# Performance work log

Measured on AMD Instinct MI355X. Metric: run time of the kernel, lower is better.

## Reference

```python
import jax, jax.numpy as jnp
import numpy as np
from jax import lax

BATCH = 524288
N_LINKS = 8   # body 0 = fixed base, bodies 1..7 have revolute joints
N_DOFS = 7
G = 9.81      # base linear acceleration z-component encodes gravity

def _skew(v):
    x, y, z = v[..., 0], v[..., 1], v[..., 2]
    o = jnp.zeros_like(x)
    return jnp.stack([jnp.stack([o, -z, y], -1),
                      jnp.stack([z, o, -x], -1),
                      jnp.stack([-y, x, o], -1)], -2)

def _rodrigues(axis, theta):
    # rotation about unit axis by theta; broadcasts axis[...,3] with theta[...]
    K = _skew(axis)
    s = jnp.sin(theta)[..., None, None]
    c = jnp.cos(theta)[..., None, None]
    I = jnp.eye(3, dtype=jnp.result_type(theta))
    return I + s * K + (1.0 - c) * (K @ K)

def setup_inputs():
    key = jax.random.key(0)
    ks = jax.random.split(key, 10)
    q = jax.random.normal(ks[0], (BATCH, N_DOFS), jnp.float32)
    qd = jax.random.normal(ks[1], (BATCH, N_DOFS), jnp.float32)
    qdd_des = jax.random.normal(ks[2], (BATCH, N_DOFS), jnp.float32)
    # fixed (URDF) joint transforms: valid random rotations + link-offset translations
    ax = jax.random.normal(ks[3], (N_LINKS, 3), jnp.float32)
    ax = ax / jnp.linalg.norm(ax, axis=-1, keepdims=True)
    ang = jax.random.uniform(ks[4], (N_LINKS,), jnp.float32, -1.0, 1.0)
    rot_fix = _rodrigues(ax, ang)
    trans_fix = jax.random.uniform(ks[5], (N_LINKS, 3), jnp.float32, -0.25, 0.25)
    # single-coordinate joint axes with signs, as in URDF revolute joints
    joint_axes = jnp.asarray([[0, 0, 1], [0, 1, 0], [0, 0, 1], [0, -1, 0],
                              [0, 0, 1], [0, 1, 0], [0, 0, 1]], jnp.float32)
    mass = jax.random.uniform(ks[6], (N_LINKS,), jnp.float32, 0.5, 4.0)
    com = 0.05 * jax.random.normal(ks[7], (N_LINKS, 3), jnp.float32)
    A = 0.1 * jax.random.normal(ks[8], (N_LINKS, 3, 3), jnp.float32)
    inertia = A @ jnp.swapaxes(A, -1, -2) + 0.05 * jnp.eye(3, dtype=jnp.float32)
    damping = jax.random.uniform(ks[9], (N_DOFS,), jnp.float32, 0.01, 0.2)
    return dict(q=q, qd=qd, qdd_des=qdd_des, rot_fix=rot_fix, trans_fix=trans_fix,
                joint_axes=joint_axes, mass=mass, com=com, inertia=inertia, damping=damping)

def reference(q, qd, qdd_des, rot_fix, trans_fix, joint_axes, mass, com, inertia, damping):
    # Batched recursive Newton-Euler inverse dynamics over a serial chain,
    # matching DifferentiableRobotModel.compute_inverse_dynamics (gravity+damping on).
    B, D = q.shape
    # joint pose of body i(=dof j+1): rotation = rot_fix[i] @ R(axis_j, q_j), translation = trans_fix[i]
    Rq = _rodrigues(joint_axes[None, :, :], q)                     # [B,D,3,3]
    R = jnp.einsum('dij,bdjk->dbik', rot_fix[1:], Rq)              # [D,B,3,3]
    p = trans_fix[1:]                                              # [D,3]
    jv = qd.T[:, :, None] * joint_axes[:, None, :]                 # [D,B,3] joint angular vel
    ja = qdd_des.T[:, :, None] * joint_axes[:, None, :]            # [D,B,3] joint angular acc

    z = jnp.zeros((B, 3), q.dtype)
    base_acc_lin = z.at[:, 2].set(G)

    # forward pass: propagate spatial velocity/acceleration root -> leaf
    def fwd_step(carry, xs):
        vl, va, al, aa = carry
        Ri, pi, jvi, jai = xs
        Rt = jnp.swapaxes(Ri, -1, -2)
        pinv = -jnp.einsum('bij,j->bi', Rt, pi)
        # SpatialMotionVec.transform with inverse joint pose (Rt, pinv)
        va_n = jnp.einsum('bij,bj->bi', Rt, va)
        vl_n = jnp.einsum('bij,bj->bi', Rt, vl) + jnp.cross(pinv, va_n)
        va_i = va_n + jvi
        vl_i = vl_n
        aa_n = jnp.einsum('bij,bj->bi', Rt, aa)
        al_n = jnp.einsum('bij,bj->bi', Rt, al) + jnp.cross(pinv, aa_n)
        # acc = parent_acc(transformed) + joint_acc + vel x joint_vel (joint_vel.lin = 0)
        aa_i = aa_n + jai + jnp.cross(va_i, jvi)
        al_i = al_n + jnp.cross(vl_i, jvi)
        new = (vl_i, va_i, al_i, aa_i)
        return new, new

    _, (vl, va, al, aa) = lax.scan(fwd_step, (z, z, base_acc_lin, z), (R, p, jv, ja))

    # spatial inertia (about body frame origin) acting on motion vectors
    m = mass[1:, None, None]                                       # [D,1,1]
    mc = mass[1:, None] * com[1:]                                  # [D,3]
    cs = _skew(com[1:])
    Io = inertia[1:] + mass[1:, None, None] * (cs @ jnp.swapaxes(cs, -1, -2))

    def imul(lin, ang):
        return (m * lin + jnp.cross(ang, mc[:, None, :]),
                jnp.einsum('dij,dbj->dbi', Io, ang) + jnp.cross(mc[:, None, :], lin))

    Ia_l, Ia_a = imul(al, aa)
    Iv_l, Iv_a = imul(vl, va)
    # f = I*acc + vel x* (I*vel)
    f_l = Ia_l + jnp.cross(va, Iv_l)
    f_a = Ia_a + jnp.cross(va, Iv_a) + jnp.cross(vl, Iv_l)

    # backward pass: accumulate forces leaf -> root; tau_j = f.ang . axis_j
    def bwd_step(carry, xs):
        cl, ca = carry
        fl, fa, Ri, pi, axi = xs
        tl = fl + cl
        ta = fa + ca
        tau = jnp.einsum('bi,i->b', ta, axi)
        # SpatialForceVec.transform with joint pose (Ri, pi)
        nl = jnp.einsum('bij,bj->bi', Ri, tl)
        na = jnp.einsum('bij,bj->bi', Ri, ta) + jnp.cross(pi[None, :], nl)
        return (nl, na), tau

    _, taus = lax.scan(bwd_step, (z, z), (f_l, f_a, R, p, joint_axes), reverse=True)
    return jnp.swapaxes(taus, 0, 1) + damping[None, :] * qd        # [B,D]
```

## Files before the change

kernel.cpp:

```cpp
#include <hip/hip_runtime.h>

#define NDOF 7
#define BLK 256
#define CST_STRIDE 24
#define CST_TOT (NDOF * CST_STRIDE)
#define NPARK 5
#define FREC 33

struct V3 { float x, y, z; };
__device__ __forceinline__ V3 operator+(V3 a, V3 b) { return {a.x + b.x, a.y + b.y, a.z + b.z}; }
__device__ __forceinline__ V3 operator-(V3 a, V3 b) { return {a.x - b.x, a.y - b.y, a.z - b.z}; }
__device__ __forceinline__ V3 operator*(float s, V3 a) { return {s * a.x, s * a.y, s * a.z}; }
__device__ __forceinline__ V3 cross(V3 a, V3 b) {
    return {a.y * b.z - a.z * b.y, a.z * b.x - a.x * b.z, a.x * b.y - a.y * b.x};
}
__device__ __forceinline__ float dot(V3 a, V3 b) { return a.x * b.x + a.y * b.y + a.z * b.z; }

__global__ void rnea_prep(const float* __restrict__ rot_fix,
                          const float* __restrict__ trans_fix,
                          const float* __restrict__ mass_g,
                          const float* __restrict__ com_g,
                          const float* __restrict__ inertia_g,
                          const float* __restrict__ damping_g,
                          float* __restrict__ cst) {
    const int d = threadIdx.x;
    if (d >= NDOF) return;
    float* o = cst + d * CST_STRIDE;
    const float* F = rot_fix + (1 + d) * 9;
#pragma unroll
    for (int j = 0; j < 3; j++)
#pragma unroll
        for (int i = 0; i < 3; i++) o[j * 3 + i] = F[i * 3 + j];
#pragma unroll
    for (int i = 0; i < 3; i++) o[9 + i] = trans_fix[(1 + d) * 3 + i];
    const float m = mass_g[1 + d];
    const float c0 = com_g[(1 + d) * 3 + 0];
    const float c1 = com_g[(1 + d) * 3 + 1];
    const float c2 = com_g[(1 + d) * 3 + 2];
    const float* I = inertia_g + (1 + d) * 9;
    o[12] = I[0] + m * (c1 * c1 + c2 * c2);
    o[13] = I[1] - m * c0 * c1;
    o[14] = I[2] - m * c0 * c2;
    o[15] = I[4] + m * (c0 * c0 + c2 * c2);
    o[16] = I[5] - m * c1 * c2;
    o[17] = I[8] + m * (c0 * c0 + c1 * c1);
    o[18] = m;
    o[19] = m * c0;
    o[20] = m * c1;
    o[21] = m * c2;
    o[22] = damping_g[d];
    o[23] = 0.f;
}

template <int AX>
__device__ __forceinline__ void make_R(V3 Fc0, V3 Fc1, V3 Fc2, float s, float c,
                                       V3& R0, V3& R1, V3& R2) {
    if (AX == 0) {
        R0 = c * Fc0 + s * Fc1;
        R1 = c * Fc1 - s * Fc0;
        R2 = Fc2;
    } else if (AX == 1) {
        R0 = c * Fc0 - s * Fc2;
        R1 = Fc1;
        R2 = s * Fc0 + c * Fc2;
    } else {
        R0 = c * Fc0 + s * Fc2;
        R1 = Fc1;
        R2 = c * Fc2 - s * Fc0;
    }
}

template <int AX>
__device__ __forceinline__ void fwd_step(const float4* C4, float s, float c,
                                         float qd, float qdd, V3& vl, V3& va, V3& al,
                                         V3& aa, V3& fl, V3& fa) {
    const float4 A0 = C4[0], A1 = C4[1], A2 = C4[2], A3 = C4[3], A4 = C4[4], A5 = C4[5];
    const V3 Fc0{A0.x, A0.y, A0.z};
    const V3 Fc1{A0.w, A1.x, A1.y};
    const V3 Fc2{A1.z, A1.w, A2.x};
    const V3 p{A2.y, A2.z, A2.w};
    const float I00 = A3.x, I01 = A3.y, I02 = A3.z, I11 = A3.w, I12 = A4.x, I22 = A4.y;
    const float m = A4.z;
    const V3 mc{A4.w, A5.x, A5.y};

    V3 R0, R1, R2;
    make_R<AX>(Fc0, Fc1, Fc2, s, c, R0, R1, R2);

    V3 w1 = vl + cross(va, p);
    V3 w2 = al + cross(aa, p);
    V3 nvl{dot(R0, w1), dot(R1, w1), dot(R2, w1)};
    V3 nva{dot(R0, va), dot(R1, va), dot(R2, va)};
    V3 nal{dot(R0, w2), dot(R1, w2), dot(R2, w2)};
    V3 naa{dot(R0, aa), dot(R1, aa), dot(R2, aa)};

    if (AX == 0) {
        va = {nva.x, nva.y, nva.z + qd};
        aa = {naa.x + va.y * qd, naa.y - va.x * qd, naa.z + qdd};
        vl = nvl;
        al = {nal.x + vl.y * qd, nal.y - vl.x * qd, nal.z};
    } else if (AX == 1) {
        va = {nva.x, nva.y + qd, nva.z};
        aa = {naa.x - va.z * qd, naa.y + qdd, naa.z + va.x * qd};
        vl = nvl;
        al = {nal.x - vl.z * qd, nal.y, nal.z + vl.x * qd};
    } else {
        va = {nva.x, nva.y - qd, nva.z};
        aa = {naa.x + va.z * qd, naa.y - qdd, naa.z - va.x * qd};
        vl = nvl;
        al = {nal.x + vl.z * qd, nal.y, nal.z - vl.x * qd};
    }

    V3 Ial = m * al + cross(aa, mc);
    V3 Iaa = V3{I00 * aa.x + I01 * aa.y + I02 * aa.z,
                I01 * aa.x + I11 * aa.y + I12 * aa.z,
                I02 * aa.x + I12 * aa.y + I22 * aa.z} + cross(mc, al);
    V3 Ivl = m * vl + cross(va, mc);
    V3 Iva = V3{I00 * va.x + I01 * va.y + I02 * va.z,
                I01 * va.x + I11 * va.y + I12 * va.z,
                I02 * va.x + I12 * va.y + I22 * va.z} + cross(mc, vl);
    fl = Ial + cross(va, Ivl);
    fa = Iaa + cross(va, Iva) + cross(vl, Ivl);
}

template <int AX>
__device__ __forceinline__ float bwd_core(const float4* C4, float s, float c,
                                          V3 fl, V3 fa, V3& cl, V3& ca) {
    const float4 A0 = C4[0], A1 = C4[1], A2 = C4[2];
    const V3 Fc0{A0.x, A0.y, A0.z};
    const V3 Fc1{A0.w, A1.x, A1.y};
    const V3 Fc2{A1.z, A1.w, A2.x};
    const V3 p{A2.y, A2.z, A2.w};

    V3 tl = fl + cl;
    V3 ta = fa + ca;
    float tau;
    if (AX == 0) tau = ta.z;
    else if (AX == 1) tau = ta.y;
    else tau = -ta.y;

    V3 R0, R1, R2;
    make_R<AX>(Fc0, Fc1, Fc2, s, c, R0, R1, R2);
    V3 nl = tl.x * R0 + tl.y * R1 + tl.z * R2;
    V3 na = ta.x * R0 + ta.y * R1 + ta.z * R2 + cross(p, nl);
    cl = nl;
    ca = na;
    return tau;
}

__global__ __launch_bounds__(BLK) void rnea_main(
    const float* __restrict__ q_g, const float* __restrict__ qd_g,
    const float* __restrict__ qdd_g, const float* __restrict__ cst,
    float* __restrict__ out, int nbatch) {
    __shared__ __align__(16) float sC[CST_TOT];
    __shared__ float sF[BLK * FREC];
    const int t = threadIdx.x;
    const int row = blockIdx.x * BLK + t;

    if (t < CST_TOT) sC[t] = cst[t];
    __syncthreads();

    const bool ok = row < nbatch;
    const size_t go = (size_t)row * NDOF;
    float qd[NDOF], ss[NDOF], cc[NDOF];
    V3 cl{0.f, 0.f, 0.f}, ca{0.f, 0.f, 0.f};
    float tau5 = 0.f, tau6 = 0.f;
    float* frec = sF + t * FREC;
    const float4* C4 = reinterpret_cast<const float4*>(sC);

    if (ok) {
        float q[NDOF], qdd[NDOF];
#pragma unroll
        for (int d = 0; d < NDOF; d++) q[d] = q_g[go + d];
#pragma unroll
        for (int d = 0; d < NDOF; d++) qd[d] = qd_g[go + d];
#pragma unroll
        for (int d = 0; d < NDOF; d++) qdd[d] = qdd_g[go + d];
#pragma unroll
        for (int d = 0; d < NDOF; d++) { ss[d] = __sinf(q[d]); cc[d] = __cosf(q[d]); }

        V3 vl{0.f, 0.f, 0.f}, va{0.f, 0.f, 0.f}, al{0.f, 0.f, 9.81f}, aa{0.f, 0.f, 0.f};
        V3 fl, fa;
        fwd_step<0>(C4 + 0 * 6, ss[0], cc[0], qd[0], qdd[0], vl, va, al, aa, fl, fa);
        frec[0] = fl.x; frec[1] = fl.y; frec[2] = fl.z; frec[3] = fa.x; frec[4] = fa.y; frec[5] = fa.z;
        fwd_step<1>(C4 + 1 * 6, ss[1], cc[1], qd[1], qdd[1], vl, va, al, aa, fl, fa);
        frec[6] = fl.x; frec[7] = fl.y; frec[8] = fl.z; frec[9] = fa.x; frec[10] = fa.y; frec[11] = fa.z;
        fwd_step<0>(C4 + 2 * 6, ss[2], cc[2], qd[2], qdd[2], vl, va, al, aa, fl, fa);
        frec[12] = fl.x; frec[13] = fl.y; frec[14] = fl.z; frec[15] = fa.x; frec[16] = fa.y; frec[17] = fa.z;
        fwd_step<2>(C4 + 3 * 6, ss[3], cc[3], qd[3], qdd[3], vl, va, al, aa, fl, fa);
        frec[18] = fl.x; frec[19] = fl.y; frec[20] = fl.z; frec[21] = fa.x; frec[22] = fa.y; frec[23] = fa.z;
        fwd_step<0>(C4 + 4 * 6, ss[4], cc[4], qd[4], qdd[4], vl, va, al, aa, fl, fa);
        frec[24] = fl.x; frec[25] = fl.y; frec[26] = fl.z; frec[27] = fa.x; frec[28] = fa.y; frec[29] = fa.z;

        V3 fl5, fa5, fl6, fa6;
        fwd_step<1>(C4 + 5 * 6, ss[5], cc[5], qd[5], qdd[5], vl, va, al, aa, fl5, fa5);
        fwd_step<0>(C4 + 6 * 6, ss[6], cc[6], qd[6], qdd[6], vl, va, al, aa, fl6, fa6);
        tau6 = bwd_core<0>(C4 + 6 * 6, ss[6], cc[6], fl6, fa6, cl, ca);
        tau5 = bwd_core<1>(C4 + 5 * 6, ss[5], cc[5], fl5, fa5, cl, ca);
    }

    __syncthreads();

    if (ok) {
        float tau[NDOF];
        tau[6] = tau6;
        tau[5] = tau5;
        V3 fl, fa;
        fl = {frec[24], frec[25], frec[26]}; fa = {frec[27], frec[28], frec[29]};
        tau[4] = bwd_core<0>(C4 + 4 * 6, ss[4], cc[4], fl, fa, cl, ca);
        fl = {frec[18], frec[19], frec[20]}; fa = {frec[21], frec[22], frec[23]};
        tau[3] = bwd_core<2>(C4 + 3 * 6, ss[3], cc[3], fl, fa, cl, ca);
        fl = {frec[12], frec[13], frec[14]}; fa = {frec[15], frec[16], frec[17]};
        tau[2] = bwd_core<0>(C4 + 2 * 6, ss[2], cc[2], fl, fa, cl, ca);
        fl = {frec[6], frec[7], frec[8]}; fa = {frec[9], frec[10], frec[11]};
        tau[1] = bwd_core<1>(C4 + 1 * 6, ss[1], cc[1], fl, fa, cl, ca);
        fl = {frec[0], frec[1], frec[2]}; fa = {frec[3], frec[4], frec[5]};
        tau[0] = bwd_core<0>(C4 + 0 * 6, ss[0], cc[0], fl, fa, cl, ca);

#pragma unroll
        for (int d = 0; d < NDOF; d++)
            out[go + d] = tau[d] + sC[d * CST_STRIDE + 22] * qd[d];
    }
}

extern "C" void kernel_launch(void* const* d_in, const int* in_sizes, int n_in,
                              void* d_out, int out_size, void* d_ws, size_t ws_size,
                              hipStream_t stream) {
    const float* q = (const float*)d_in[0];
    const float* qd = (const float*)d_in[1];
    const float* qdd = (const float*)d_in[2];
    const float* rot_fix = (const float*)d_in[3];
    const float* trans_fix = (const float*)d_in[4];
    const float* mass = (const float*)d_in[6];
    const float* com = (const float*)d_in[7];
    const float* inertia = (const float*)d_in[8];
    const float* damping = (const float*)d_in[9];
    float* out = (float*)d_out;
    float* cst = (float*)d_ws;

    const int n_elem = in_sizes[0];
    const int B = n_elem / NDOF;
    const int grid = (B + BLK - 1) / BLK;

    rnea_prep<<<1, 64, 0, stream>>>(rot_fix, trans_fix, mass, com, inertia, damping, cst);
    rnea_main<<<grid, BLK, 0, stream>>>(q, qd, qdd, cst, out, B);
}
```

Measured before the change: 123.4 us.

## Replace stored-force backward pass with eager per-link force propagation

Each link's spatial force is now propagated toward the root as soon as the forward step produces it, and its contribution is added to every ancestor's torque. This removes the per-thread shared-memory record of forces (about 33 KB per block), so occupancy can rise. The cost is quadratic work: 21 transform steps instead of 7. The separate prep kernel is also merged into the main kernel, with each block computing the link constants into shared memory, which drops one launch.

Measured after the change: 148.0 us. 1.2x slower.

```diff
diff --git a/kernel.cpp b/kernel.cpp
--- a/kernel.cpp
+++ b/kernel.cpp
@@ -4,8 +4,6 @@
 #define BLK 256
 #define CST_STRIDE 24
 #define CST_TOT (NDOF * CST_STRIDE)
-#define NPARK 5
-#define FREC 33
 
 struct V3 { float x, y, z; };
 __device__ __forceinline__ V3 operator+(V3 a, V3 b) { return {a.x + b.x, a.y + b.y, a.z + b.z}; }
@@ -15,42 +13,6 @@
     return {a.y * b.z - a.z * b.y, a.z * b.x - a.x * b.z, a.x * b.y - a.y * b.x};
 }
 __device__ __forceinline__ float dot(V3 a, V3 b) { return a.x * b.x + a.y * b.y + a.z * b.z; }
-
-__global__ void rnea_prep(const float* __restrict__ rot_fix,
-                          const float* __restrict__ trans_fix,
-                          const float* __restrict__ mass_g,
-                          const float* __restrict__ com_g,
-                          const float* __restrict__ inertia_g,
-                          const float* __restrict__ damping_g,
-                          float* __restrict__ cst) {
-    const int d = threadIdx.x;
-    if (d >= NDOF) return;
-    float* o = cst + d * CST_STRIDE;
-    const float* F = rot_fix + (1 + d) * 9;
-#pragma unroll
-    for (int j = 0; j < 3; j++)
-#pragma unroll
-        for (int i = 0; i < 3; i++) o[j * 3 + i] = F[i * 3 + j];
-#pragma unroll
-    for (int i = 0; i < 3; i++) o[9 + i] = trans_fix[(1 + d) * 3 + i];
-    const float m = mass_g[1 + d];
-    const float c0 = com_g[(1 + d) * 3 + 0];
-    const float c1 = com_g[(1 + d) * 3 + 1];
-    const float c2 = com_g[(1 + d) * 3 + 2];
-    const float* I = inertia_g + (1 + d) * 9;
-    o[12] = I[0] + m * (c1 * c1 + c2 * c2);
-    o[13] = I[1] - m * c0 * c1;
-    o[14] = I[2] - m * c0 * c2;
-    o[15] = I[4] + m * (c0 * c0 + c2 * c2);
-    o[16] = I[5] - m * c1 * c2;
-    o[17] = I[8] + m * (c0 * c0 + c1 * c1);
-    o[18] = m;
-    o[19] = m * c0;
-    o[20] = m * c1;
-    o[21] = m * c2;
-    o[22] = damping_g[d];
-    o[23] = 0.f;
-}
 
 template <int AX>
 __device__ __forceinline__ void make_R(V3 Fc0, V3 Fc1, V3 Fc2, float s, float c,
@@ -123,52 +85,73 @@
 }
 
 template <int AX>
-__device__ __forceinline__ float bwd_core(const float4* C4, float s, float c,
-                                          V3 fl, V3 fa, V3& cl, V3& ca) {
+__device__ __forceinline__ void prop_step(const float4* C4, float s, float c,
+                                          V3& tl, V3& ta) {
     const float4 A0 = C4[0], A1 = C4[1], A2 = C4[2];
     const V3 Fc0{A0.x, A0.y, A0.z};
     const V3 Fc1{A0.w, A1.x, A1.y};
     const V3 Fc2{A1.z, A1.w, A2.x};
     const V3 p{A2.y, A2.z, A2.w};
-
-    V3 tl = fl + cl;
-    V3 ta = fa + ca;
-    float tau;
-    if (AX == 0) tau = ta.z;
-    else if (AX == 1) tau = ta.y;
-    else tau = -ta.y;
-
     V3 R0, R1, R2;
     make_R<AX>(Fc0, Fc1, Fc2, s, c, R0, R1, R2);
     V3 nl = tl.x * R0 + tl.y * R1 + tl.z * R2;
     V3 na = ta.x * R0 + ta.y * R1 + ta.z * R2 + cross(p, nl);
-    cl = nl;
-    ca = na;
-    return tau;
+    tl = nl;
+    ta = na;
+}
+
+template <int AX>
+__device__ __forceinline__ float taudot(V3 ta) {
+    if (AX == 0) return ta.z;
+    else if (AX == 1) return ta.y;
+    else return -ta.y;
 }
 
 __global__ __launch_bounds__(BLK) void rnea_main(
     const float* __restrict__ q_g, const float* __restrict__ qd_g,
-    const float* __restrict__ qdd_g, const float* __restrict__ cst,
+    const float* __restrict__ qdd_g,
+    const float* __restrict__ rot_fix, const float* __restrict__ trans_fix,
+    const float* __restrict__ mass_g, const float* __restrict__ com_g,
+    const float* __restrict__ inertia_g, const float* __restrict__ damping_g,
     float* __restrict__ out, int nbatch) {
     __shared__ __align__(16) float sC[CST_TOT];
-    __shared__ float sF[BLK * FREC];
     const int t = threadIdx.x;
     const int row = blockIdx.x * BLK + t;
-
-    if (t < CST_TOT) sC[t] = cst[t];
-    __syncthreads();
-
     const bool ok = row < nbatch;
     const size_t go = (size_t)row * NDOF;
-    float qd[NDOF], ss[NDOF], cc[NDOF];
-    V3 cl{0.f, 0.f, 0.f}, ca{0.f, 0.f, 0.f};
-    float tau5 = 0.f, tau6 = 0.f;
-    float* frec = sF + t * FREC;
-    const float4* C4 = reinterpret_cast<const float4*>(sC);
-
+
+    if (t < NDOF) {
+        const int d = t;
+        float* o = sC + d * CST_STRIDE;
+        const float* F = rot_fix + (1 + d) * 9;
+#pragma unroll
+        for (int j = 0; j < 3; j++)
+#pragma unroll
+            for (int i = 0; i < 3; i++) o[j * 3 + i] = F[i * 3 + j];
+#pragma unroll
+        for (int i = 0; i < 3; i++) o[9 + i] = trans_fix[(1 + d) * 3 + i];
+        const float m = mass_g[1 + d];
+        const float c0 = com_g[(1 + d) * 3 + 0];
+        const float c1 = com_g[(1 + d) * 3 + 1];
+        const float c2 = com_g[(1 + d) * 3 + 2];
+        const float* I = inertia_g + (1 + d) * 9;
+        o[12] = I[0] + m * (c1 * c1 + c2 * c2);
+        o[13] = I[1] - m * c0 * c1;
+        o[14] = I[2] - m * c0 * c2;
+        o[15] = I[4] + m * (c0 * c0 + c2 * c2);
+        o[16] = I[5] - m * c1 * c2;
+        o[17] = I[8] + m * (c0 * c0 + c1 * c1);
+        o[18] = m;
+        o[19] = m * c0;
+        o[20] = m * c1;
+        o[21] = m * c2;
+        o[22] = damping_g[d];
+        o[23] = 0.f;
+    }
+
+    float qd[NDOF], ss[NDOF], cc[NDOF], qdd[NDOF];
     if (ok) {
-        float q[NDOF], qdd[NDOF];
+        float q[NDOF];
 #pragma unroll
         for (int d = 0; d < NDOF; d++) q[d] = q_g[go + d];
 #pragma unroll
@@ -177,45 +160,65 @@
         for (int d = 0; d < NDOF; d++) qdd[d] = qdd_g[go + d];
 #pragma unroll
         for (int d = 0; d < NDOF; d++) { ss[d] = __sinf(q[d]); cc[d] = __cosf(q[d]); }
-
+    }
+
+    __syncthreads();
+
+    if (ok) {
+        const float4* C4 = reinterpret_cast<const float4*>(sC);
         V3 vl{0.f, 0.f, 0.f}, va{0.f, 0.f, 0.f}, al{0.f, 0.f, 9.81f}, aa{0.f, 0.f, 0.f};
-        V3 fl, fa;
+        V3 fl, fa, tl, ta;
+        float tau0, tau1, tau2, tau3, tau4, tau5, tau6;
+
         fwd_step<0>(C4 + 0 * 6, ss[0], cc[0], qd[0], qdd[0], vl, va, al, aa, fl, fa);
-        frec[0] = fl.x; frec[1] = fl.y; frec[2] = fl.z; frec[3] = fa.x; frec[4] = fa.y; frec[5] = fa.z;
+        tau0 = taudot<0>(fa);
+
         fwd_step<1>(C4 + 1 * 6, ss[1], cc[1], qd[1], qdd[1], vl, va, al, aa, fl, fa);
-        frec[6] = fl.x; frec[7] = fl.y; frec[8] = fl.z; frec[9] = fa.x; frec[10] = fa.y; frec[11] = fa.z;
+        tau1 = taudot<1>(fa);
+        tl = fl; ta = fa;
+        prop_step<1>(C4 + 1 * 6, ss[1], cc[1], tl, ta); tau0 += taudot<0>(ta);
+
         fwd_step<0>(C4 + 2 * 6, ss[2], cc[2], qd[2], qdd[2], vl, va, al, aa, fl, fa);
-        frec[12] = fl.x; frec[13] = fl.y; frec[14] = fl.z; frec[15] = fa.x; frec[16] = fa.y; frec[17] = fa.z;
+        tau2 = taudot<0>(fa);
+        tl = fl; ta = fa;
+        prop_step<0>(C4 + 2 * 6, ss[2], cc[2], tl, ta); tau1 += taudot<1>(ta);
+        prop_step<1>(C4 + 1 * 6, ss[1], cc[1], tl, ta); tau0 += taudot<0>(ta);
+
         fwd_step<2>(C4 + 3 * 6, ss[3], cc[3], qd[3], qdd[3], vl, va, al, aa, fl, fa);
-        frec[18] = fl.x; frec[19] = fl.y; frec[20] = fl.z; frec[21] = fa.x; frec[22] = fa.y; frec[23] = fa.z;
+        tau3 = taudot<2>(fa);
+        tl = fl; ta = fa;
+        prop_step<2>(C4 + 3 * 6, ss[3], cc[3], tl, ta); tau2 += taudot<0>(ta);
+        prop_step<0>(C4 + 2 * 6, ss[2], cc[2], tl, ta); tau1 += taudot<1>(ta);
+        prop_step<1>(C4 + 1 * 6, ss[1], cc[1], tl, ta); tau0 += taudot<0>(ta);
+
         fwd_step<0>(C4 + 4 * 6, ss[4], cc[4], qd[4], qdd[4], vl, va, al, aa, fl, fa);
-        frec[24] = fl.x; frec[25] = fl.y; frec[26] = fl.z; frec[27] = fa.x; frec[28] = fa.y; frec[29] = fa.z;
-
-        V3 fl5, fa5, fl6, fa6;
-        fwd_step<1>(C4 + 5 * 6, ss[5], cc[5], qd[5], qdd[5], vl, va, al, aa, fl5, fa5);
-        fwd_step<0>(C4 + 6 * 6, ss[6], cc[6], qd[6], qdd[6], vl, va, al, aa, fl6, fa6);
-        tau6 = bwd_core<0>(C4 + 6 * 6, ss[6], cc[6], fl6, fa6, cl, ca);
-        tau5 = bwd_core<1>(C4 + 5 * 6, ss[5], cc[5], fl5, fa5, cl, ca);
-    }
-
-    __syncthreads();
-
-    if (ok) {
-        float tau[NDOF];
-        tau[6] = tau6;
-        tau[5] = tau5;
-        V3 fl, fa;
-        fl = {frec[24], frec[25], frec[26]}; fa = {frec[27], frec[28], frec[29]};
-        tau[4] = bwd_core<0>(C4 + 4 * 6, ss[4], cc[4], fl, fa, cl, ca);
-        fl = {frec[18], frec[19], frec[20]}; fa = {frec[21], frec[22], frec[23]};
-        tau[3] = bwd_core<2>(C4 + 3 * 6, ss[3], cc[3], fl, fa, cl, ca);
-        fl = {frec[12], frec[13], frec[14]}; fa = {frec[15], frec[16], frec[17]};
-        tau[2] = bwd_core<0>(C4 + 2 * 6, ss[2], cc[2], fl, fa, cl, ca);
-        fl = {frec[6], frec[7], frec[8]}; fa = {frec[9], frec[10], frec[11]};
-        tau[1] = bwd_core<1>(C4 + 1 * 6, ss[1], cc[1], fl, fa, cl, ca);
-        fl = {frec[0], frec[1], frec[2]}; fa = {frec[3], frec[4], frec[5]};
-        tau[0] = bwd_core<0>(C4 + 0 * 6, ss[0], cc[0], fl, fa, cl, ca);
-
+        tau4 = taudot<0>(fa);
+        tl = fl; ta = fa;
+        prop_step<0>(C4 + 4 * 6, ss[4], cc[4], tl, ta); tau3 += taudot<2>(ta);
+        prop_step<2>(C4 + 3 * 6, ss[3], cc[3], tl, ta); tau2 += taudot<0>(ta);
+        prop_step<0>(C4 + 2 * 6, ss[2], cc[2], tl, ta); tau1 += taudot<1>(ta);
+        prop_step<1>(C4 + 1 * 6, ss[1], cc[1], tl, ta); tau0 += taudot<0>(ta);
+
+        fwd_step<1>(C4 + 5 * 6, ss[5], cc[5], qd[5], qdd[5], vl, va, al, aa, fl, fa);
+        tau5 = taudot<1>(fa);
+        tl = fl; ta = fa;
+        prop_step<1>(C4 + 5 * 6, ss[5], cc[5], tl, ta); tau4 += taudot<0>(ta);
+        prop_step<0>(C4 + 4 * 6, ss[4], cc[4], tl, ta); tau3 += taudot<2>(ta);
+        prop_step<2>(C4 + 3 * 6, ss[3], cc[3], tl, ta); tau2 += taudot<0>(ta);
+        prop_step<0>(C4 + 2 * 6, ss[2], cc[2], tl, ta); tau1 += taudot<1>(ta);
+        prop_step<1>(C4 + 1 * 6, ss[1], cc[1], tl, ta); tau0 += taudot<0>(ta);
+
+        fwd_step<0>(C4 + 6 * 6, ss[6], cc[6], qd[6], qdd[6], vl, va, al, aa, fl, fa);
+        tau6 = taudot<0>(fa);
+        tl = fl; ta = fa;
+        prop_step<0>(C4 + 6 * 6, ss[6], cc[6], tl, ta); tau5 += taudot<1>(ta);
+        prop_step<1>(C4 + 5 * 6, ss[5], cc[5], tl, ta); tau4 += taudot<0>(ta);
+        prop_step<0>(C4 + 4 * 6, ss[4], cc[4], tl, ta); tau3 += taudot<2>(ta);
+        prop_step<2>(C4 + 3 * 6, ss[3], cc[3], tl, ta); tau2 += taudot<0>(ta);
+        prop_step<0>(C4 + 2 * 6, ss[2], cc[2], tl, ta); tau1 += taudot<1>(ta);
+        prop_step<1>(C4 + 1 * 6, ss[1], cc[1], tl, ta); tau0 += taudot<0>(ta);
+
+        float tau[NDOF] = {tau0, tau1, tau2, tau3, tau4, tau5, tau6};
 #pragma unroll
         for (int d = 0; d < NDOF; d++)
             out[go + d] = tau[d] + sC[d * CST_STRIDE + 22] * qd[d];
@@ -235,12 +238,11 @@
     const float* inertia = (const float*)d_in[8];
     const float* damping = (const float*)d_in[9];
     float* out = (float*)d_out;
-    float* cst = (float*)d_ws;
 
     const int n_elem = in_sizes[0];
     const int B = n_elem / NDOF;
     const int grid = (B + BLK - 1) / BLK;
 
-    rnea_prep<<<1, 64, 0, stream>>>(rot_fix, trans_fix, mass, com, inertia, damping, cst);
-    rnea_main<<<grid, BLK, 0, stream>>>(q, qd, qdd, cst, out, B);
-}
+    rnea_main<<<grid, BLK, 0, stream>>>(q, qd, qdd, rot_fix, trans_fix, mass, com,
+                                        inertia, damping, out, B);
+}
```

## Keep forward forces in registers and read constants directly from global memory

Applied to the files above, without the earlier changes.

Removes the shared-memory staging of the per-link constants and the per-thread shared-memory spill of forward-pass forces. All seven links' spatial forces now stay in registers, and constants are read through uniform global loads that the compiler can turn into scalar loads. This drops the LDS traffic and both block barriers, and clamps out-of-range rows instead of branching around the compute. The cost is higher VGPR pressure, which may lower occupancy or cause spills.

Result: slower. 134.5 us (+9.0%).

```diff
diff --git a/kernel.cpp b/kernel.cpp
--- a/kernel.cpp
+++ b/kernel.cpp
@@ -4,8 +4,6 @@
 #define BLK 256
 #define CST_STRIDE 24
 #define CST_TOT (NDOF * CST_STRIDE)
-#define NPARK 5
-#define FREC 33
 
 struct V3 { float x, y, z; };
 __device__ __forceinline__ V3 operator+(V3 a, V3 b) { return {a.x + b.x, a.y + b.y, a.z + b.z}; }
@@ -71,17 +69,16 @@
 }
 
 template <int AX>
-__device__ __forceinline__ void fwd_step(const float4* C4, float s, float c,
+__device__ __forceinline__ void fwd_step(const float* __restrict__ C, float s, float c,
                                          float qd, float qdd, V3& vl, V3& va, V3& al,
                                          V3& aa, V3& fl, V3& fa) {
-    const float4 A0 = C4[0], A1 = C4[1], A2 = C4[2], A3 = C4[3], A4 = C4[4], A5 = C4[5];
-    const V3 Fc0{A0.x, A0.y, A0.z};
-    const V3 Fc1{A0.w, A1.x, A1.y};
-    const V3 Fc2{A1.z, A1.w, A2.x};
-    const V3 p{A2.y, A2.z, A2.w};
-    const float I00 = A3.x, I01 = A3.y, I02 = A3.z, I11 = A3.w, I12 = A4.x, I22 = A4.y;
-    const float m = A4.z;
-    const V3 mc{A4.w, A5.x, A5.y};
+    const V3 Fc0{C[0], C[1], C[2]};
+    const V3 Fc1{C[3], C[4], C[5]};
+    const V3 Fc2{C[6], C[7], C[8]};
+    const V3 p{C[9], C[10], C[11]};
+    const float I00 = C[12], I01 = C[13], I02 = C[14], I11 = C[15], I12 = C[16], I22 = C[17];
+    const float m = C[18];
+    const V3 mc{C[19], C[20], C[21]};
 
     V3 R0, R1, R2;
     make_R<AX>(Fc0, Fc1, Fc2, s, c, R0, R1, R2);
@@ -123,13 +120,12 @@
 }
 
 template <int AX>
-__device__ __forceinline__ float bwd_core(const float4* C4, float s, float c,
+__device__ __forceinline__ float bwd_core(const float* __restrict__ C, float s, float c,
                                           V3 fl, V3 fa, V3& cl, V3& ca) {
-    const float4 A0 = C4[0], A1 = C4[1], A2 = C4[2];
-    const V3 Fc0{A0.x, A0.y, A0.z};
-    const V3 Fc1{A0.w, A1.x, A1.y};
-    const V3 Fc2{A1.z, A1.w, A2.x};
-    const V3 p{A2.y, A2.z, A2.w};
+    const V3 Fc0{C[0], C[1], C[2]};
+    const V3 Fc1{C[3], C[4], C[5]};
+    const V3 Fc2{C[6], C[7], C[8]};
+    const V3 p{C[9], C[10], C[11]};
 
     V3 tl = fl + cl;
     V3 ta = fa + ca;
@@ -151,74 +147,46 @@
     const float* __restrict__ q_g, const float* __restrict__ qd_g,
     const float* __restrict__ qdd_g, const float* __restrict__ cst,
     float* __restrict__ out, int nbatch) {
-    __shared__ __align__(16) float sC[CST_TOT];
-    __shared__ float sF[BLK * FREC];
     const int t = threadIdx.x;
     const int row = blockIdx.x * BLK + t;
-
-    if (t < CST_TOT) sC[t] = cst[t];
-    __syncthreads();
-
-    const bool ok = row < nbatch;
-    const size_t go = (size_t)row * NDOF;
-    float qd[NDOF], ss[NDOF], cc[NDOF];
+    const int rowc = row < nbatch ? row : (nbatch - 1);
+    const size_t go = (size_t)rowc * NDOF;
+
+    float q[NDOF], qd[NDOF], qdd[NDOF], ss[NDOF], cc[NDOF];
+#pragma unroll
+    for (int d = 0; d < NDOF; d++) q[d] = q_g[go + d];
+#pragma unroll
+    for (int d = 0; d < NDOF; d++) qd[d] = qd_g[go + d];
+#pragma unroll
+    for (int d = 0; d < NDOF; d++) qdd[d] = qdd_g[go + d];
+#pragma unroll
+    for (int d = 0; d < NDOF; d++) { ss[d] = __sinf(q[d]); cc[d] = __cosf(q[d]); }
+
+    V3 vl{0.f, 0.f, 0.f}, va{0.f, 0.f, 0.f}, al{0.f, 0.f, 9.81f}, aa{0.f, 0.f, 0.f};
+    V3 fl0, fa0, fl1, fa1, fl2, fa2, fl3, fa3, fl4, fa4, fl5, fa5, fl6, fa6;
+
+    fwd_step<0>(cst + 0 * CST_STRIDE, ss[0], cc[0], qd[0], qdd[0], vl, va, al, aa, fl0, fa0);
+    fwd_step<1>(cst + 1 * CST_STRIDE, ss[1], cc[1], qd[1], qdd[1], vl, va, al, aa, fl1, fa1);
+    fwd_step<0>(cst + 2 * CST_STRIDE, ss[2], cc[2], qd[2], qdd[2], vl, va, al, aa, fl2, fa2);
+    fwd_step<2>(cst + 3 * CST_STRIDE, ss[3], cc[3], qd[3], qdd[3], vl, va, al, aa, fl3, fa3);
+    fwd_step<0>(cst + 4 * CST_STRIDE, ss[4], cc[4], qd[4], qdd[4], vl, va, al, aa, fl4, fa4);
+    fwd_step<1>(cst + 5 * CST_STRIDE, ss[5], cc[5], qd[5], qdd[5], vl, va, al, aa, fl5, fa5);
+    fwd_step<0>(cst + 6 * CST_STRIDE, ss[6], cc[6], qd[6], qdd[6], vl, va, al, aa, fl6, fa6);
+
     V3 cl{0.f, 0.f, 0.f}, ca{0.f, 0.f, 0.f};
-    float tau5 = 0.f, tau6 = 0.f;
-    float* frec = sF + t * FREC;
-    const float4* C4 = reinterpret_cast<const float4*>(sC);
-
-    if (ok) {
-        float q[NDOF], qdd[NDOF];
-#pragma unroll
-        for (int d = 0; d < NDOF; d++) q[d] = q_g[go + d];
-#pragma unroll
-        for (int d = 0; d < NDOF; d++) qd[d] = qd_g[go + d];
-#pragma unroll
-        for (int d = 0; d < NDOF; d++) qdd[d] = qdd_g[go + d];
-#pragma unroll
-        for (int d = 0; d < NDOF; d++) { ss[d] = __sinf(q[d]); cc[d] = __cosf(q[d]); }
-
-        V3 vl{0.f, 0.f, 0.f}, va{0.f, 0.f, 0.f}, al{0.f, 0.f, 9.81f}, aa{0.f, 0.f, 0.f};
-        V3 fl, fa;
-        fwd_step<0>(C4 + 0 * 6, ss[0], cc[0], qd[0], qdd[0], vl, va, al, aa, fl, fa);
-        frec[0] = fl.x; frec[1] = fl.y; frec[2] = fl.z; frec[3] = fa.x; frec[4] = fa.y; frec[5] = fa.z;
-        fwd_step<1>(C4 + 1 * 6, ss[1], cc[1], qd[1], qdd[1], vl, va, al, aa, fl, fa);
-        frec[6] = fl.x; frec[7] = fl.y; frec[8] = fl.z; frec[9] = fa.x; frec[10] = fa.y; frec[11] = fa.z;
-        fwd_step<0>(C4 + 2 * 6, ss[2], cc[2], qd[2], qdd[2], vl, va, al, aa, fl, fa);
-        frec[12] = fl.x; frec[13] = fl.y; frec[14] = fl.z; frec[15] = fa.x; frec[16] = fa.y; frec[17] = fa.z;
-        fwd_step<2>(C4 + 3 * 6, ss[3], cc[3], qd[3], qdd[3], vl, va, al, aa, fl, fa);
-        frec[18] = fl.x; frec[19] = fl.y; frec[20] = fl.z; frec[21] = fa.x; frec[22] = fa.y; frec[23] = fa.z;
-        fwd_step<0>(C4 + 4 * 6, ss[4], cc[4], qd[4], qdd[4], vl, va, al, aa, fl, fa);
-        frec[24] = fl.x; frec[25] = fl.y; frec[26] = fl.z; frec[27] = fa.x; frec[28] = fa.y; frec[29] = fa.z;
-
-        V3 fl5, fa5, fl6, fa6;
-        fwd_step<1>(C4 + 5 * 6, ss[5], cc[5], qd[5], qdd[5], vl, va, al, aa, fl5, fa5);
-        fwd_step<0>(C4 + 6 * 6, ss[6], cc[6], qd[6], qdd[6], vl, va, al, aa, fl6, fa6);
-        tau6 = bwd_core<0>(C4 + 6 * 6, ss[6], cc[6], fl6, fa6, cl, ca);
-        tau5 = bwd_core<1>(C4 + 5 * 6, ss[5], cc[5], fl5, fa5, cl, ca);
-    }
-
-    __syncthreads();
-
-    if (ok) {
-        float tau[NDOF];
-        tau[6] = tau6;
-        tau[5] = tau5;
-        V3 fl, fa;
-        fl = {frec[24], frec[25], frec[26]}; fa = {frec[27], frec[28], frec[29]};
-        tau[4] = bwd_core<0>(C4 + 4 * 6, ss[4], cc[4], fl, fa, cl, ca);
-        fl = {frec[18], frec[19], frec[20]}; fa = {frec[21], frec[22], frec[23]};
-        tau[3] = bwd_core<2>(C4 + 3 * 6, ss[3], cc[3], fl, fa, cl, ca);
-        fl = {frec[12], frec[13], frec[14]}; fa = {frec[15], frec[16], frec[17]};
-        tau[2] = bwd_core<0>(C4 + 2 * 6, ss[2], cc[2], fl, fa, cl, ca);
-        fl = {frec[6], frec[7], frec[8]}; fa = {frec[9], frec[10], frec[11]};
-        tau[1] = bwd_core<1>(C4 + 1 * 6, ss[1], cc[1], fl, fa, cl, ca);
-        fl = {frec[0], frec[1], frec[2]}; fa = {frec[3], frec[4], frec[5]};
-        tau[0] = bwd_core<0>(C4 + 0 * 6, ss[0], cc[0], fl, fa, cl, ca);
-
+    float tau[NDOF];
+    tau[6] = bwd_core<0>(cst + 6 * CST_STRIDE, ss[6], cc[6], fl6, fa6, cl, ca);
+    tau[5] = bwd_core<1>(cst + 5 * CST_STRIDE, ss[5], cc[5], fl5, fa5, cl, ca);
+    tau[4] = bwd_core<0>(cst + 4 * CST_STRIDE, ss[4], cc[4], fl4, fa4, cl, ca);
+    tau[3] = bwd_core<2>(cst + 3 * CST_STRIDE, ss[3], cc[3], fl3, fa3, cl, ca);
+    tau[2] = bwd_core<0>(cst + 2 * CST_STRIDE, ss[2], cc[2], fl2, fa2, cl, ca);
+    tau[1] = bwd_core<1>(cst + 1 * CST_STRIDE, ss[1], cc[1], fl1, fa1, cl, ca);
+    tau[0] = bwd_core<0>(cst + 0 * CST_STRIDE, ss[0], cc[0], fl0, fa0, cl, ca);
+
+    if (row < nbatch) {
 #pragma unroll
         for (int d = 0; d < NDOF; d++)
-            out[go + d] = tau[d] + sC[d * CST_STRIDE + 22] * qd[d];
+            out[go + d] = tau[d] + cst[d * CST_STRIDE + 22] * qd[d];
     }
 }
 
```

## Fuse constant prep into main kernel and roll RNEA loops with SoA force spill

Applied to the files above, without the earlier changes.

Removes the separate prep kernel so each block computes the per-link constants into shared memory, saving one launch. The forward and backward recursions become non-unrolled loops with a runtime axis switch. All seven link forces are spilled to a structure-of-arrays shared buffer to avoid bank conflicts, and q/qd are reloaded and sin/cos recomputed in the backward pass instead of being held in registers. This aims to cut register pressure and raise occupancy, at the cost of extra global reloads, duplicated transcendental work, branch overhead and a larger shared-memory footprint.

New measurement: 126.8 us. 2.7% more time.

```diff
diff --git a/kernel.cpp b/kernel.cpp
--- a/kernel.cpp
+++ b/kernel.cpp
@@ -4,8 +4,7 @@
 #define BLK 256
 #define CST_STRIDE 24
 #define CST_TOT (NDOF * CST_STRIDE)
-#define NPARK 5
-#define FREC 33
+#define SF_FLOATS (NDOF * 6 * BLK)
 
 struct V3 { float x, y, z; };
 __device__ __forceinline__ V3 operator+(V3 a, V3 b) { return {a.x + b.x, a.y + b.y, a.z + b.z}; }
@@ -15,42 +14,6 @@
     return {a.y * b.z - a.z * b.y, a.z * b.x - a.x * b.z, a.x * b.y - a.y * b.x};
 }
 __device__ __forceinline__ float dot(V3 a, V3 b) { return a.x * b.x + a.y * b.y + a.z * b.z; }
-
-__global__ void rnea_prep(const float* __restrict__ rot_fix,
-                          const float* __restrict__ trans_fix,
-                          const float* __restrict__ mass_g,
-                          const float* __restrict__ com_g,
-                          const float* __restrict__ inertia_g,
-                          const float* __restrict__ damping_g,
-                          float* __restrict__ cst) {
-    const int d = threadIdx.x;
-    if (d >= NDOF) return;
-    float* o = cst + d * CST_STRIDE;
-    const float* F = rot_fix + (1 + d) * 9;
-#pragma unroll
-    for (int j = 0; j < 3; j++)
-#pragma unroll
-        for (int i = 0; i < 3; i++) o[j * 3 + i] = F[i * 3 + j];
-#pragma unroll
-    for (int i = 0; i < 3; i++) o[9 + i] = trans_fix[(1 + d) * 3 + i];
-    const float m = mass_g[1 + d];
-    const float c0 = com_g[(1 + d) * 3 + 0];
-    const float c1 = com_g[(1 + d) * 3 + 1];
-    const float c2 = com_g[(1 + d) * 3 + 2];
-    const float* I = inertia_g + (1 + d) * 9;
-    o[12] = I[0] + m * (c1 * c1 + c2 * c2);
-    o[13] = I[1] - m * c0 * c1;
-    o[14] = I[2] - m * c0 * c2;
-    o[15] = I[4] + m * (c0 * c0 + c2 * c2);
-    o[16] = I[5] - m * c1 * c2;
-    o[17] = I[8] + m * (c0 * c0 + c1 * c1);
-    o[18] = m;
-    o[19] = m * c0;
-    o[20] = m * c1;
-    o[21] = m * c2;
-    o[22] = damping_g[d];
-    o[23] = 0.f;
-}
 
 template <int AX>
 __device__ __forceinline__ void make_R(V3 Fc0, V3 Fc1, V3 Fc2, float s, float c,
@@ -147,78 +110,92 @@
     return tau;
 }
 
+__device__ __forceinline__ int axid(int d) { return (d & 1) ? ((d == 3) ? 2 : 1) : 0; }
+
 __global__ __launch_bounds__(BLK) void rnea_main(
     const float* __restrict__ q_g, const float* __restrict__ qd_g,
-    const float* __restrict__ qdd_g, const float* __restrict__ cst,
+    const float* __restrict__ qdd_g,
+    const float* __restrict__ rot_fix, const float* __restrict__ trans_fix,
+    const float* __restrict__ mass_g, const float* __restrict__ com_g,
+    const float* __restrict__ inertia_g, const float* __restrict__ damping_g,
     float* __restrict__ out, int nbatch) {
     __shared__ __align__(16) float sC[CST_TOT];
-    __shared__ float sF[BLK * FREC];
+    __shared__ float sF[SF_FLOATS];
     const int t = threadIdx.x;
     const int row = blockIdx.x * BLK + t;
-
-    if (t < CST_TOT) sC[t] = cst[t];
+    const bool ok = row < nbatch;
+    const int rc = ok ? row : (nbatch - 1);
+    const size_t go = (size_t)rc * NDOF;
+
+    if (t < NDOF) {
+        const int d = t;
+        float* o = sC + d * CST_STRIDE;
+        const float* F = rot_fix + (1 + d) * 9;
+#pragma unroll
+        for (int j = 0; j < 3; j++)
+#pragma unroll
+            for (int i = 0; i < 3; i++) o[j * 3 + i] = F[i * 3 + j];
+#pragma unroll
+        for (int i = 0; i < 3; i++) o[9 + i] = trans_fix[(1 + d) * 3 + i];
+        const float m = mass_g[1 + d];
+        const float c0 = com_g[(1 + d) * 3 + 0];
+        const float c1 = com_g[(1 + d) * 3 + 1];
+        const float c2 = com_g[(1 + d) * 3 + 2];
+        const float* I = inertia_g + (1 + d) * 9;
+        o[12] = I[0] + m * (c1 * c1 + c2 * c2);
+        o[13] = I[1] - m * c0 * c1;
+        o[14] = I[2] - m * c0 * c2;
+        o[15] = I[4] + m * (c0 * c0 + c2 * c2);
+        o[16] = I[5] - m * c1 * c2;
+        o[17] = I[8] + m * (c0 * c0 + c1 * c1);
+        o[18] = m;
+        o[19] = m * c0;
+        o[20] = m * c1;
+        o[21] = m * c2;
+        o[22] = damping_g[d];
+        o[23] = 0.f;
+    }
     __syncthreads();
 
-    const bool ok = row < nbatch;
-    const size_t go = (size_t)row * NDOF;
-    float qd[NDOF], ss[NDOF], cc[NDOF];
+    V3 vl{0.f, 0.f, 0.f}, va{0.f, 0.f, 0.f}, al{0.f, 0.f, 9.81f}, aa{0.f, 0.f, 0.f};
+    float q_n = q_g[go], qd_n = qd_g[go], qdd_n = qdd_g[go];
+#pragma clang loop unroll(disable)
+    for (int d = 0; d < NDOF; ++d) {
+        const float qc = q_n, qdc = qd_n, qddc = qdd_n;
+        const int dn = (d < NDOF - 1) ? (d + 1) : (NDOF - 1);
+        q_n = q_g[go + dn];
+        qd_n = qd_g[go + dn];
+        qdd_n = qdd_g[go + dn];
+        const float s = __sinf(qc), c = __cosf(qc);
+        const float4* C4 = reinterpret_cast<const float4*>(sC) + d * 6;
+        V3 fl, fa;
+        switch (axid(d)) {
+            case 0: fwd_step<0>(C4, s, c, qdc, qddc, vl, va, al, aa, fl, fa); break;
+            case 1: fwd_step<1>(C4, s, c, qdc, qddc, vl, va, al, aa, fl, fa); break;
+            default: fwd_step<2>(C4, s, c, qdc, qddc, vl, va, al, aa, fl, fa); break;
+        }
+        float* r = sF + d * 6 * BLK + t;
+        r[0 * BLK] = fl.x; r[1 * BLK] = fl.y; r[2 * BLK] = fl.z;
+        r[3 * BLK] = fa.x; r[4 * BLK] = fa.y; r[5 * BLK] = fa.z;
+    }
+
     V3 cl{0.f, 0.f, 0.f}, ca{0.f, 0.f, 0.f};
-    float tau5 = 0.f, tau6 = 0.f;
-    float* frec = sF + t * FREC;
-    const float4* C4 = reinterpret_cast<const float4*>(sC);
-
-    if (ok) {
-        float q[NDOF], qdd[NDOF];
-#pragma unroll
-        for (int d = 0; d < NDOF; d++) q[d] = q_g[go + d];
-#pragma unroll
-        for (int d = 0; d < NDOF; d++) qd[d] = qd_g[go + d];
-#pragma unroll
-        for (int d = 0; d < NDOF; d++) qdd[d] = qdd_g[go + d];
-#pragma unroll
-        for (int d = 0; d < NDOF; d++) { ss[d] = __sinf(q[d]); cc[d] = __cosf(q[d]); }
-
-        V3 vl{0.f, 0.f, 0.f}, va{0.f, 0.f, 0.f}, al{0.f, 0.f, 9.81f}, aa{0.f, 0.f, 0.f};
-        V3 fl, fa;
-        fwd_step<0>(C4 + 0 * 6, ss[0], cc[0], qd[0], qdd[0], vl, va, al, aa, fl, fa);
-        frec[0] = fl.x; frec[1] = fl.y; frec[2] = fl.z; frec[3] = fa.x; frec[4] = fa.y; frec[5] = fa.z;
-        fwd_step<1>(C4 + 1 * 6, ss[1], cc[1], qd[1], qdd[1], vl, va, al, aa, fl, fa);
-        frec[6] = fl.x; frec[7] = fl.y; frec[8] = fl.z; frec[9] = fa.x; frec[10] = fa.y; frec[11] = fa.z;
-        fwd_step<0>(C4 + 2 * 6, ss[2], cc[2], qd[2], qdd[2], vl, va, al, aa, fl, fa);
-        frec[12] = fl.x; frec[13] = fl.y; frec[14] = fl.z; frec[15] = fa.x; frec[16] = fa.y; frec[17] = fa.z;
-        fwd_step<2>(C4 + 3 * 6, ss[3], cc[3], qd[3], qdd[3], vl, va, al, aa, fl, fa);
-        frec[18] = fl.x; frec[19] = fl.y; frec[20] = fl.z; frec[21] = fa.x; frec[22] = fa.y; frec[23] = fa.z;
-        fwd_step<0>(C4 + 4 * 6, ss[4], cc[4], qd[4], qdd[4], vl, va, al, aa, fl, fa);
-        frec[24] = fl.x; frec[25] = fl.y; frec[26] = fl.z; frec[27] = fa.x; frec[28] = fa.y; frec[29] = fa.z;
-
-        V3 fl5, fa5, fl6, fa6;
-        fwd_step<1>(C4 + 5 * 6, ss[5], cc[5], qd[5], qdd[5], vl, va, al, aa, fl5, fa5);
-        fwd_step<0>(C4 + 6 * 6, ss[6], cc[6], qd[6], qdd[6], vl, va, al, aa, fl6, fa6);
-        tau6 = bwd_core<0>(C4 + 6 * 6, ss[6], cc[6], fl6, fa6, cl, ca);
-        tau5 = bwd_core<1>(C4 + 5 * 6, ss[5], cc[5], fl5, fa5, cl, ca);
-    }
-
-    __syncthreads();
-
-    if (ok) {
-        float tau[NDOF];
-        tau[6] = tau6;
-        tau[5] = tau5;
-        V3 fl, fa;
-        fl = {frec[24], frec[25], frec[26]}; fa = {frec[27], frec[28], frec[29]};
-        tau[4] = bwd_core<0>(C4 + 4 * 6, ss[4], cc[4], fl, fa, cl, ca);
-        fl = {frec[18], frec[19], frec[20]}; fa = {frec[21], frec[22], frec[23]};
-        tau[3] = bwd_core<2>(C4 + 3 * 6, ss[3], cc[3], fl, fa, cl, ca);
-        fl = {frec[12], frec[13], frec[14]}; fa = {frec[15], frec[16], frec[17]};
-        tau[2] = bwd_core<0>(C4 + 2 * 6, ss[2], cc[2], fl, fa, cl, ca);
-        fl = {frec[6], frec[7], frec[8]}; fa = {frec[9], frec[10], frec[11]};
-        tau[1] = bwd_core<1>(C4 + 1 * 6, ss[1], cc[1], fl, fa, cl, ca);
-        fl = {frec[0], frec[1], frec[2]}; fa = {frec[3], frec[4], frec[5]};
-        tau[0] = bwd_core<0>(C4 + 0 * 6, ss[0], cc[0], fl, fa, cl, ca);
-
-#pragma unroll
-        for (int d = 0; d < NDOF; d++)
-            out[go + d] = tau[d] + sC[d * CST_STRIDE + 22] * qd[d];
+#pragma clang loop unroll(disable)
+    for (int d = NDOF - 1; d >= 0; --d) {
+        const float qc = q_g[go + d];
+        const float qdc = qd_g[go + d];
+        const float s = __sinf(qc), c = __cosf(qc);
+        const float4* C4 = reinterpret_cast<const float4*>(sC) + d * 6;
+        const float* r = sF + d * 6 * BLK + t;
+        const V3 fl{r[0 * BLK], r[1 * BLK], r[2 * BLK]};
+        const V3 fa{r[3 * BLK], r[4 * BLK], r[5 * BLK]};
+        float tau;
+        switch (axid(d)) {
+            case 0: tau = bwd_core<0>(C4, s, c, fl, fa, cl, ca); break;
+            case 1: tau = bwd_core<1>(C4, s, c, fl, fa, cl, ca); break;
+            default: tau = bwd_core<2>(C4, s, c, fl, fa, cl, ca); break;
+        }
+        if (ok) out[go + d] = tau + sC[d * CST_STRIDE + 22] * qdc;
     }
 }
 
@@ -235,12 +212,11 @@
     const float* inertia = (const float*)d_in[8];
     const float* damping = (const float*)d_in[9];
     float* out = (float*)d_out;
-    float* cst = (float*)d_ws;
 
     const int n_elem = in_sizes[0];
     const int B = n_elem / NDOF;
     const int grid = (B + BLK - 1) / BLK;
 
-    rnea_prep<<<1, 64, 0, stream>>>(rot_fix, trans_fix, mass, com, inertia, damping, cst);
-    rnea_main<<<grid, BLK, 0, stream>>>(q, qd, qdd, cst, out, B);
-}
+    rnea_main<<<grid, BLK, 0, stream>>>(q, qd, qdd, rot_fix, trans_fix, mass, com,
+                                        inertia, damping, out, B);
+}
```
